# Kernel tuning notes

Measured on AMD Instinct MI355X. Metric: run time of the kernel, lower is better.

## Reference

```python
import jax, jax.numpy as jnp
import numpy as np

D = 256
NODE_COUNTS = [200000, 50000, 12000, 4000]  # n_src per block; dst of block l = NODE_COUNTS[l+1]
EDGE_COUNTS = [500000, 120000, 40000]


def setup_inputs() -> dict:
    key = jax.random.key(0)
    ks = jax.random.split(key, 16)
    x = jax.random.normal(ks[0], (NODE_COUNTS[0], D), dtype=jnp.float32)
    inp = {"x": x}
    scale = 1.0 / np.sqrt(D)
    ki = 1
    for l in range(3):
        inp[f"Wself{l}"] = jax.random.normal(ks[ki], (D, D), dtype=jnp.float32) * scale; ki += 1
        inp[f"Wneigh{l}"] = jax.random.normal(ks[ki], (D, D), dtype=jnp.float32) * scale; ki += 1
        inp[f"b{l}"] = jnp.zeros((D,), dtype=jnp.float32)
    for l in range(3):
        e = EDGE_COUNTS[l]
        inp[f"src{l}"] = jax.random.randint(ks[ki], (e,), 0, NODE_COUNTS[l]); ki += 1
        inp[f"dst{l}"] = jax.random.randint(ks[ki], (e,), 0, NODE_COUNTS[l + 1]); ki += 1
    inp["nd0"], inp["nd1"], inp["nd2"] = NODE_COUNTS[1], NODE_COUNTS[2], NODE_COUNTS[3]
    return inp


def _sage_layer(h, src, dst, n_dst, Ws, Wn, b, relu=True):
    # DGL SAGEConv('mean'): out = fc_self(h_dst) + fc_neigh(mean_{u in N(v)} h_u) + bias
    h_dst = h[:n_dst]
    msgs = h[src]                                               # [E, d] gather
    agg = jax.ops.segment_sum(msgs, dst, num_segments=n_dst)    # [n_dst, d]
    deg = jax.ops.segment_sum(jnp.ones((dst.shape[0],), h.dtype), dst, num_segments=n_dst)
    mean = agg / jnp.maximum(deg, 1.0)[:, None]
    out = h_dst @ Ws + mean @ Wn + b
    return jax.nn.relu(out) if relu else out


def reference(x, Wself0, Wneigh0, b0, Wself1, Wneigh1, b1, Wself2, Wneigh2, b2,
              src0, dst0, src1, dst1, src2, dst2, nd0, nd1, nd2):
    h = _sage_layer(x, src0, dst0, nd0, Wself0, Wneigh0, b0)
    h = _sage_layer(h, src1, dst1, nd1, Wself1, Wneigh1, b1)
    h = _sage_layer(h, src2, dst2, nd2, Wself2, Wneigh2, b2)
    return h
```

## Files before the change

### kernel.cpp

```cpp
#include <hip/hip_runtime.h>
#include <stdint.h>

#define D 256

typedef __attribute__((ext_vector_type(8))) short bf16x8;
typedef __attribute__((ext_vector_type(4))) float f32x4;

__device__ inline unsigned short f2bf(float f) {
    union { float f; uint32_t u; } v; v.f = f;
    return (unsigned short)((v.u + 0x7FFFu + ((v.u >> 16) & 1u)) >> 16);
}
__device__ inline float bf2f(unsigned short b) {
    return __uint_as_float(((uint32_t)b) << 16);
}

#define SEG0 0
#define SEG1 50176
#define SEG2 62464
#define CURTOT 66560
#define NBLK 65

__global__ __launch_bounds__(256) void convert_rows(
    const float* __restrict__ in, unsigned short* __restrict__ out, long n8)
{
    long t = (long)blockIdx.x * 256 + threadIdx.x;
    if (t >= n8) return;
    const float4* p = (const float4*)in + t * 2;
    float4 a = p[0], b = p[1];
    unsigned short r[8] = {f2bf(a.x), f2bf(a.y), f2bf(a.z), f2bf(a.w),
                           f2bf(b.x), f2bf(b.y), f2bf(b.z), f2bf(b.w)};
    *(uint4*)(out + t * 8) = *(uint4*)r;
}

struct WPtrs { const float* w[6]; };
__global__ __launch_bounds__(256) void convert_weights(
    WPtrs wp, unsigned short* __restrict__ out)
{
    int t = blockIdx.x * 256 + threadIdx.x;
    int m = t >> 16, e = t & 65535;
    int col = e >> 8, k = e & 255;
    out[t] = f2bf(wp.w[m][(k << 8) + col]);
}

__global__ __launch_bounds__(256) void count_all(
    const int* __restrict__ d0, const int* __restrict__ d1, const int* __restrict__ d2,
    int* __restrict__ cur, int E0, int E01, int Etot)
{
    int e = blockIdx.x * 256 + threadIdx.x;
    if (e >= Etot) return;
    int base, d;
    if (e < E0)       { base = SEG0; d = d0[e]; }
    else if (e < E01) { base = SEG1; d = d1[e - E0]; }
    else              { base = SEG2; d = d2[e - E01]; }
    atomicAdd(&cur[base + d], 1);
}

__global__ __launch_bounds__(256) void scan_blocks(
    int* __restrict__ cur, int* __restrict__ bsum)
{
    __shared__ int wsum[4];
    int tid = threadIdx.x, lane = tid & 63, wid = tid >> 6;
    int base = blockIdx.x * 1024 + tid * 4;
    int4 v = *(int4*)(cur + base);
    int t0 = v.x, t01 = t0 + v.y, t012 = t01 + v.z, tot = t012 + v.w;
    int incl = tot;
    #pragma unroll
    for (int ofs = 1; ofs < 64; ofs <<= 1) {
        int t = __shfl_up(incl, ofs, 64);
        if (lane >= ofs) incl += t;
    }
    if (lane == 63) wsum[wid] = incl;
    __syncthreads();
    if (tid == 0) {
        int run = 0;
        #pragma unroll
        for (int w = 0; w < 4; ++w) { int t = wsum[w]; wsum[w] = run; run += t; }
        bsum[blockIdx.x] = run;
    }
    __syncthreads();
    int texcl = wsum[wid] + incl - tot;
    v.x = texcl; v.y = texcl + t0; v.z = texcl + t01; v.w = texcl + t012;
    *(int4*)(cur + base) = v;
}

__global__ __launch_bounds__(128) void scan_bsums(
    const int* __restrict__ bsum, int* __restrict__ bscan)
{
    __shared__ int s[NBLK];
    int tid = threadIdx.x;
    if (tid < NBLK) s[tid] = bsum[tid];
    __syncthreads();
    if (tid == 0) {
        int run = 0;
        for (int b = 0; b < 49; ++b)  { int t = s[b]; s[b] = run; run += t; }
        run = 0;
        for (int b = 49; b < 61; ++b) { int t = s[b]; s[b] = run; run += t; }
        run = 0;
        for (int b = 61; b < 65; ++b) { int t = s[b]; s[b] = run; run += t; }
    }
    __syncthreads();
    if (tid < NBLK) bscan[tid] = s[tid];
}

__global__ __launch_bounds__(256) void scan_addback(
    int* __restrict__ cur, const int* __restrict__ bscan)
{
    int base = blockIdx.x * 1024 + threadIdx.x * 4;
    int add = bscan[blockIdx.x];
    int4 v = *(int4*)(cur + base);
    v.x += add; v.y += add; v.z += add; v.w += add;
    *(int4*)(cur + base) = v;
}

__global__ __launch_bounds__(256) void fill_all(
    const int* __restrict__ s0, const int* __restrict__ s1, const int* __restrict__ s2,
    const int* __restrict__ d0, const int* __restrict__ d1, const int* __restrict__ d2,
    int* __restrict__ cur, int* __restrict__ idx, int E0, int E01, int Etot)
{
    int e = blockIdx.x * 256 + threadIdx.x;
    if (e >= Etot) return;
    int base, d, s, ib;
    if (e < E0)       { base = SEG0; d = d0[e];       s = s0[e];       ib = 0; }
    else if (e < E01) { base = SEG1; d = d1[e - E0];  s = s1[e - E0];  ib = E0; }
    else              { base = SEG2; d = d2[e - E01]; s = s2[e - E01]; ib = E01; }
    int p = atomicAdd(&cur[base + d], 1);
    idx[ib + p] = s;
}

template<int BF16IN>
__global__ __launch_bounds__(256) void gather_mean_k(
    const void* __restrict__ hv, const int* __restrict__ idx,
    const int* __restrict__ curseg, unsigned short* __restrict__ mean, int M)
{
    int t = blockIdx.x * blockDim.x + threadIdx.x;
    int w = t >> 6, lane = t & 63;
    if (w >= M) return;
    int e0 = w ? curseg[w - 1] : 0;
    int e1 = curseg[w];
    float4 acc = make_float4(0.f, 0.f, 0.f, 0.f);
    int e = e0;
    if (BF16IN) {
        const unsigned short* h = (const unsigned short*)hv;
        for (; e + 1 < e1; e += 2) {
            int sa = idx[e], sb = idx[e + 1];
            ushort4 va = *(const ushort4*)(h + (size_t)sa * D + lane * 4);
            ushort4 vb = *(const ushort4*)(h + (size_t)sb * D + lane * 4);
            acc.x += bf2f(va.x) + bf2f(vb.x);
            acc.y += bf2f(va.y) + bf2f(vb.y);
            acc.z += bf2f(va.z) + bf2f(vb.z);
            acc.w += bf2f(va.w) + bf2f(vb.w);
        }
        if (e < e1) {
            int sa = idx[e];
            ushort4 va = *(const ushort4*)(h + (size_t)sa * D + lane * 4);
            acc.x += bf2f(va.x); acc.y += bf2f(va.y);
            acc.z += bf2f(va.z); acc.w += bf2f(va.w);
        }
    } else {
        const float* h = (const float*)hv;
        for (; e + 1 < e1; e += 2) {
            int sa = idx[e], sb = idx[e + 1];
            float4 va = *((const float4*)(h + (size_t)sa * D) + lane);
            float4 vb = *((const float4*)(h + (size_t)sb * D) + lane);
            acc.x += va.x + vb.x; acc.y += va.y + vb.y;
            acc.z += va.z + vb.z; acc.w += va.w + vb.w;
        }
        if (e < e1) {
            int sa = idx[e];
            float4 va = *((const float4*)(h + (size_t)sa * D) + lane);
            acc.x += va.x; acc.y += va.y; acc.z += va.z; acc.w += va.w;
        }
    }
    float r = 1.0f / fmaxf((float)(e1 - e0), 1.0f);
    ushort4 o;
    o.x = f2bf(acc.x * r); o.y = f2bf(acc.y * r);
    o.z = f2bf(acc.z * r); o.w = f2bf(acc.w * r);
    *(ushort4*)(mean + (size_t)w * D + lane * 4) = o;
}

template<int FINAL>
__global__ __launch_bounds__(256) void sage_gemm_mfma(
    const unsigned short* __restrict__ A1,
    const unsigned short* __restrict__ A2,
    const unsigned short* __restrict__ Wt1,
    const unsigned short* __restrict__ Wt2,
    const float* __restrict__ bias,
    void* __restrict__ outv,
    int M)
{
    __shared__ unsigned short As[128 * 32];
    __shared__ unsigned short Bs[128 * 32];

    int tid = threadIdx.x;
    int lane = tid & 63, wid = tid >> 6;
    int wr = wid >> 1, wc = wid & 1;
    int m0 = blockIdx.x * 128, n0 = blockIdx.y * 128;
    int l15 = lane & 15, lq = lane >> 4;

    f32x4 acc[4][4] = {};

    for (int kt = 0; kt < 16; ++kt) {
        const unsigned short* A = (kt < 8) ? A1 : A2;
        const unsigned short* B = (kt < 8) ? Wt1 : Wt2;
        int kk = (kt & 7) * 32;
        #pragma unroll
        for (int q = 0; q < 2; ++q) {
            int off16 = q * 256 + tid;
            int r = off16 >> 2, c16 = off16 & 3;
            int gr = m0 + r; if (gr >= M) gr = M - 1;
            const unsigned short* src = A + (size_t)gr * 256 + kk + c16 * 8;
            __builtin_amdgcn_global_load_lds(
                (const __attribute__((address_space(1))) void*)src,
                (__attribute__((address_space(3))) void*)(As + (q * 256 + wid * 64) * 8),
                16, 0, 0);
        }
        #pragma unroll
        for (int q = 0; q < 2; ++q) {
            int off16 = q * 256 + tid;
            int col = off16 >> 2, c16 = off16 & 3;
            const unsigned short* src = B + (size_t)(n0 + col) * 256 + kk + c16 * 8;
            __builtin_amdgcn_global_load_lds(
                (const __attribute__((address_space(1))) void*)src,
                (__attribute__((address_space(3))) void*)(Bs + (q * 256 + wid * 64) * 8),
                16, 0, 0);
        }
        __syncthreads();

        bf16x8 af[4], bfr[4];
        #pragma unroll
        for (int i = 0; i < 4; ++i) {
            int row = wr * 64 + i * 16 + l15;
            af[i] = *(const bf16x8*)(As + row * 32 + lq * 8);
            int col = wc * 64 + i * 16 + l15;
            bfr[i] = *(const bf16x8*)(Bs + col * 32 + lq * 8);
        }
        #pragma unroll
        for (int mr = 0; mr < 4; ++mr)
            #pragma unroll
            for (int nc = 0; nc < 4; ++nc)
                acc[mr][nc] = __builtin_amdgcn_mfma_f32_16x16x32_bf16(
                    af[mr], bfr[nc], acc[mr][nc], 0, 0, 0);
        __syncthreads();
    }

    #pragma unroll
    for (int nc = 0; nc < 4; ++nc) {
        int gc = n0 + wc * 64 + nc * 16 + l15;
        float bv = bias[gc];
        #pragma unroll
        for (int mr = 0; mr < 4; ++mr) {
            #pragma unroll
            for (int reg = 0; reg < 4; ++reg) {
                int gr = m0 + wr * 64 + mr * 16 + lq * 4 + reg;
                if (gr < M) {
                    float v = fmaxf(acc[mr][nc][reg] + bv, 0.f);
                    if (FINAL) ((float*)outv)[(size_t)gr * 256 + gc] = v;
                    else ((unsigned short*)outv)[(size_t)gr * 256 + gc] = f2bf(v);
                }
            }
        }
    }
}

extern "C" void kernel_launch(void* const* d_in, const int* in_sizes, int n_in,
                              void* d_out, int out_size, void* d_ws, size_t ws_size,
                              hipStream_t stream) {
    const float* x = (const float*)d_in[0];
    const float* Wself[3]  = {(const float*)d_in[1], (const float*)d_in[4], (const float*)d_in[7]};
    const float* Wneigh[3] = {(const float*)d_in[2], (const float*)d_in[5], (const float*)d_in[8]};
    const float* bias[3]   = {(const float*)d_in[3], (const float*)d_in[6], (const float*)d_in[9]};
    const int* src[3] = {(const int*)d_in[10], (const int*)d_in[12], (const int*)d_in[14]};
    const int* dst[3] = {(const int*)d_in[11], (const int*)d_in[13], (const int*)d_in[15]};
    int E[3]    = {in_sizes[10], in_sizes[12], in_sizes[14]};
    int ndst[3] = {50000, 12000, 4000};
    int E0 = E[0], E01 = E[0] + E[1], Etot = E[0] + E[1] + E[2];

    unsigned short* xb    = (unsigned short*)d_ws;
    unsigned short* h1b   = xb + (size_t)50000 * D;
    unsigned short* h2b   = h1b + (size_t)50000 * D;
    unsigned short* meanb = h2b + (size_t)12000 * D;
    unsigned short* wt    = meanb + (size_t)50000 * D;
    int* cur   = (int*)(wt + 6 * 65536);
    int* bsum  = cur + CURTOT;
    int* bscan = bsum + 80;
    int* idxa  = bscan + 80;

    WPtrs wp;
    wp.w[0] = Wself[0]; wp.w[1] = Wneigh[0];
    wp.w[2] = Wself[1]; wp.w[3] = Wneigh[1];
    wp.w[4] = Wself[2]; wp.w[5] = Wneigh[2];
    convert_weights<<<(6 * 65536) / 256, 256, 0, stream>>>(wp, wt);

    long n8 = (long)50000 * D / 8;
    convert_rows<<<(unsigned)((n8 + 255) / 256), 256, 0, stream>>>(x, xb, n8);

    hipMemsetAsync(cur, 0, CURTOT * sizeof(int), stream);
    count_all<<<(Etot + 255) / 256, 256, 0, stream>>>(dst[0], dst[1], dst[2], cur, E0, E01, Etot);
    scan_blocks<<<NBLK, 256, 0, stream>>>(cur, bsum);
    scan_bsums<<<1, 128, 0, stream>>>(bsum, bscan);
    scan_addback<<<NBLK, 256, 0, stream>>>(cur, bscan);
    fill_all<<<(Etot + 255) / 256, 256, 0, stream>>>(src[0], src[1], src[2],
        dst[0], dst[1], dst[2], cur, idxa, E0, E01, Etot);

    const unsigned short* hin_b[3] = {xb, h1b, h2b};
    void* houts[3] = {h1b, h2b, d_out};
    int segb[3] = {SEG0, SEG1, SEG2};
    int idxb[3] = {0, E0, E01};

    for (int l = 0; l < 3; ++l) {
        int M = ndst[l];
        int gt = M * 64;
        if (l == 0)
            gather_mean_k<0><<<(gt + 255) / 256, 256, 0, stream>>>(
                x, idxa + idxb[l], cur + segb[l], meanb, M);
        else
            gather_mean_k<1><<<(gt + 255) / 256, 256, 0, stream>>>(
                hin_b[l], idxa + idxb[l], cur + segb[l], meanb, M);

        dim3 grid((M + 127) / 128, 2);
        if (l < 2)
            sage_gemm_mfma<0><<<grid, 256, 0, stream>>>(hin_b[l], meanb,
                wt + (size_t)(2 * l) * 65536, wt + (size_t)(2 * l + 1) * 65536,
                bias[l], houts[l], M);
        else
            sage_gemm_mfma<1><<<grid, 256, 0, stream>>>(hin_b[l], meanb,
                wt + (size_t)(2 * l) * 65536, wt + (size_t)(2 * l + 1) * 65536,
                bias[l], houts[l], M);
    }
}
```

Before: 280.2 us.

## Fuse preprocessing kernels, convert all x to bf16, widen GEMM tile to full N

Merges weight conversion, x-to-bf16 conversion and degree counting into one launch, and converts all 200000 rows of x to bf16 instead of only the first 50000. The layer-0 gather then reads bf16 rows rather than fp32, halving the gathered bytes. The GEMM now computes all 256 output columns per block with a 128x256 tile and launch_bounds(256,2), so the A tile is loaded once instead of twice. The cost is converting 150000 extra rows, more registers per thread, and half as many GEMM blocks.

```diff
diff --git a/kernel.cpp b/kernel.cpp
--- a/kernel.cpp
+++ b/kernel.cpp
@@ -20,39 +20,43 @@
 #define CURTOT 66560
 #define NBLK 65
 
-__global__ __launch_bounds__(256) void convert_rows(
-    const float* __restrict__ in, unsigned short* __restrict__ out, long n8)
-{
-    long t = (long)blockIdx.x * 256 + threadIdx.x;
-    if (t >= n8) return;
-    const float4* p = (const float4*)in + t * 2;
-    float4 a = p[0], b = p[1];
-    unsigned short r[8] = {f2bf(a.x), f2bf(a.y), f2bf(a.z), f2bf(a.w),
-                           f2bf(b.x), f2bf(b.y), f2bf(b.z), f2bf(b.w)};
-    *(uint4*)(out + t * 8) = *(uint4*)r;
-}
-
-struct WPtrs { const float* w[6]; };
-__global__ __launch_bounds__(256) void convert_weights(
-    WPtrs wp, unsigned short* __restrict__ out)
-{
-    int t = blockIdx.x * 256 + threadIdx.x;
-    int m = t >> 16, e = t & 65535;
-    int col = e >> 8, k = e & 255;
-    out[t] = f2bf(wp.w[m][(k << 8) + col]);
-}
-
-__global__ __launch_bounds__(256) void count_all(
-    const int* __restrict__ d0, const int* __restrict__ d1, const int* __restrict__ d2,
-    int* __restrict__ cur, int E0, int E01, int Etot)
-{
-    int e = blockIdx.x * 256 + threadIdx.x;
-    if (e >= Etot) return;
-    int base, d;
-    if (e < E0)       { base = SEG0; d = d0[e]; }
-    else if (e < E01) { base = SEG1; d = d1[e - E0]; }
-    else              { base = SEG2; d = d2[e - E01]; }
-    atomicAdd(&cur[base + d], 1);
+#define WBLK 1536
+#define XBLK 25000
+
+struct PreArgs {
+    const float* w[6];
+    const float* x;
+    unsigned short* wt;
+    unsigned short* xb;
+    const int* d0; const int* d1; const int* d2;
+    int* cur;
+    int E0, E01, Etot, cblk0;
+};
+
+__global__ __launch_bounds__(256) void fused_pre(PreArgs a)
+{
+    int b = blockIdx.x;
+    if (b < WBLK) {
+        int t = b * 256 + threadIdx.x;
+        int m = t >> 16, e = t & 65535;
+        int col = e >> 8, k = e & 255;
+        a.wt[t] = f2bf(a.w[m][(k << 8) + col]);
+    } else if (b < WBLK + XBLK) {
+        long t = (long)(b - WBLK) * 256 + threadIdx.x;
+        const float4* p = (const float4*)a.x + t * 2;
+        float4 v0 = p[0], v1 = p[1];
+        unsigned short r[8] = {f2bf(v0.x), f2bf(v0.y), f2bf(v0.z), f2bf(v0.w),
+                               f2bf(v1.x), f2bf(v1.y), f2bf(v1.z), f2bf(v1.w)};
+        *(uint4*)(a.xb + t * 8) = *(uint4*)r;
+    } else {
+        int e = (b - a.cblk0) * 256 + threadIdx.x;
+        if (e >= a.Etot) return;
+        int base, d;
+        if (e < a.E0)       { base = SEG0; d = a.d0[e]; }
+        else if (e < a.E01) { base = SEG1; d = a.d1[e - a.E0]; }
+        else                { base = SEG2; d = a.d2[e - a.E01]; }
+        atomicAdd(&a.cur[base + d], 1);
+    }
 }
 
 __global__ __launch_bounds__(256) void scan_blocks(
@@ -127,9 +131,8 @@
     idx[ib + p] = s;
 }
 
-template<int BF16IN>
 __global__ __launch_bounds__(256) void gather_mean_k(
-    const void* __restrict__ hv, const int* __restrict__ idx,
+    const unsigned short* __restrict__ h, const int* __restrict__ idx,
     const int* __restrict__ curseg, unsigned short* __restrict__ mean, int M)
 {
     int t = blockIdx.x * blockDim.x + threadIdx.x;
@@ -139,37 +142,20 @@
     int e1 = curseg[w];
     float4 acc = make_float4(0.f, 0.f, 0.f, 0.f);
     int e = e0;
-    if (BF16IN) {
-        const unsigned short* h = (const unsigned short*)hv;
-        for (; e + 1 < e1; e += 2) {
-            int sa = idx[e], sb = idx[e + 1];
-            ushort4 va = *(const ushort4*)(h + (size_t)sa * D + lane * 4);
-            ushort4 vb = *(const ushort4*)(h + (size_t)sb * D + lane * 4);
-            acc.x += bf2f(va.x) + bf2f(vb.x);
-            acc.y += bf2f(va.y) + bf2f(vb.y);
-            acc.z += bf2f(va.z) + bf2f(vb.z);
-            acc.w += bf2f(va.w) + bf2f(vb.w);
-        }
-        if (e < e1) {
-            int sa = idx[e];
-            ushort4 va = *(const ushort4*)(h + (size_t)sa * D + lane * 4);
-            acc.x += bf2f(va.x); acc.y += bf2f(va.y);
-            acc.z += bf2f(va.z); acc.w += bf2f(va.w);
-        }
-    } else {
-        const float* h = (const float*)hv;
-        for (; e + 1 < e1; e += 2) {
-            int sa = idx[e], sb = idx[e + 1];
-            float4 va = *((const float4*)(h + (size_t)sa * D) + lane);
-            float4 vb = *((const float4*)(h + (size_t)sb * D) + lane);
-            acc.x += va.x + vb.x; acc.y += va.y + vb.y;
-            acc.z += va.z + vb.z; acc.w += va.w + vb.w;
-        }
-        if (e < e1) {
-            int sa = idx[e];
-            float4 va = *((const float4*)(h + (size_t)sa * D) + lane);
-            acc.x += va.x; acc.y += va.y; acc.z += va.z; acc.w += va.w;
-        }
+    for (; e + 1 < e1; e += 2) {
+        int sa = idx[e], sb = idx[e + 1];
+        ushort4 va = *(const ushort4*)(h + (size_t)sa * D + lane * 4);
+        ushort4 vb = *(const ushort4*)(h + (size_t)sb * D + lane * 4);
+        acc.x += bf2f(va.x) + bf2f(vb.x);
+        acc.y += bf2f(va.y) + bf2f(vb.y);
+        acc.z += bf2f(va.z) + bf2f(vb.z);
+        acc.w += bf2f(va.w) + bf2f(vb.w);
+    }
+    if (e < e1) {
+        int sa = idx[e];
+        ushort4 va = *(const ushort4*)(h + (size_t)sa * D + lane * 4);
+        acc.x += bf2f(va.x); acc.y += bf2f(va.y);
+        acc.z += bf2f(va.z); acc.w += bf2f(va.w);
     }
     float r = 1.0f / fmaxf((float)(e1 - e0), 1.0f);
     ushort4 o;
@@ -179,7 +165,7 @@
 }
 
 template<int FINAL>
-__global__ __launch_bounds__(256) void sage_gemm_mfma(
+__global__ __launch_bounds__(256, 2) void sage_gemm_mfma(
     const unsigned short* __restrict__ A1,
     const unsigned short* __restrict__ A2,
     const unsigned short* __restrict__ Wt1,
@@ -189,15 +175,15 @@
     int M)
 {
     __shared__ unsigned short As[128 * 32];
-    __shared__ unsigned short Bs[128 * 32];
+    __shared__ unsigned short Bs[256 * 32];
 
     int tid = threadIdx.x;
     int lane = tid & 63, wid = tid >> 6;
     int wr = wid >> 1, wc = wid & 1;
-    int m0 = blockIdx.x * 128, n0 = blockIdx.y * 128;
+    int m0 = blockIdx.x * 128;
     int l15 = lane & 15, lq = lane >> 4;
 
-    f32x4 acc[4][4] = {};
+    f32x4 acc[4][8] = {};
 
     for (int kt = 0; kt < 16; ++kt) {
         const unsigned short* A = (kt < 8) ? A1 : A2;
@@ -205,8 +191,8 @@
         int kk = (kt & 7) * 32;
         #pragma unroll
         for (int q = 0; q < 2; ++q) {
-            int off16 = q * 256 + tid;
-            int r = off16 >> 2, c16 = off16 & 3;
+            int ch = q * 256 + tid;
+            int r = ch >> 2, c16 = ch & 3;
             int gr = m0 + r; if (gr >= M) gr = M - 1;
             const unsigned short* src = A + (size_t)gr * 256 + kk + c16 * 8;
             __builtin_amdgcn_global_load_lds(
@@ -215,10 +201,10 @@
                 16, 0, 0);
         }
         #pragma unroll
-        for (int q = 0; q < 2; ++q) {
-            int off16 = q * 256 + tid;
-            int col = off16 >> 2, c16 = off16 & 3;
-            const unsigned short* src = B + (size_t)(n0 + col) * 256 + kk + c16 * 8;
+        for (int q = 0; q < 4; ++q) {
+            int ch = q * 256 + tid;
+            int col = ch >> 2, c16 = ch & 3;
+            const unsigned short* src = B + (size_t)col * 256 + kk + c16 * 8;
             __builtin_amdgcn_global_load_lds(
                 (const __attribute__((address_space(1))) void*)src,
                 (__attribute__((address_space(3))) void*)(Bs + (q * 256 + wid * 64) * 8),
@@ -226,26 +212,26 @@
         }
         __syncthreads();
 
-        bf16x8 af[4], bfr[4];
-        #pragma unroll
-        for (int i = 0; i < 4; ++i) {
-            int row = wr * 64 + i * 16 + l15;
-            af[i] = *(const bf16x8*)(As + row * 32 + lq * 8);
-            int col = wc * 64 + i * 16 + l15;
-            bfr[i] = *(const bf16x8*)(Bs + col * 32 + lq * 8);
-        }
+        bf16x8 af[4], bfr[8];
+        #pragma unroll
+        for (int i = 0; i < 4; ++i)
+            af[i] = *(const bf16x8*)(As + (wr * 64 + i * 16 + l15) * 32 + lq * 8);
+        #pragma unroll
+        for (int i = 0; i < 8; ++i)
+            bfr[i] = *(const bf16x8*)(Bs + (wc * 128 + i * 16 + l15) * 32 + lq * 8);
+
         #pragma unroll
         for (int mr = 0; mr < 4; ++mr)
             #pragma unroll
-            for (int nc = 0; nc < 4; ++nc)
+            for (int nc = 0; nc < 8; ++nc)
                 acc[mr][nc] = __builtin_amdgcn_mfma_f32_16x16x32_bf16(
                     af[mr], bfr[nc], acc[mr][nc], 0, 0, 0);
         __syncthreads();
     }
 
     #pragma unroll
-    for (int nc = 0; nc < 4; ++nc) {
-        int gc = n0 + wc * 64 + nc * 16 + l15;
+    for (int nc = 0; nc < 8; ++nc) {
+        int gc = wc * 128 + nc * 16 + l15;
         float bv = bias[gc];
         #pragma unroll
         for (int mr = 0; mr < 4; ++mr) {
@@ -276,7 +262,7 @@
     int E0 = E[0], E01 = E[0] + E[1], Etot = E[0] + E[1] + E[2];
 
     unsigned short* xb    = (unsigned short*)d_ws;
-    unsigned short* h1b   = xb + (size_t)50000 * D;
+    unsigned short* h1b   = xb + (size_t)200000 * D;
     unsigned short* h2b   = h1b + (size_t)50000 * D;
     unsigned short* meanb = h2b + (size_t)12000 * D;
     unsigned short* wt    = meanb + (size_t)50000 * D;
@@ -285,17 +271,19 @@
     int* bscan = bsum + 80;
     int* idxa  = bscan + 80;
 
-    WPtrs wp;
-    wp.w[0] = Wself[0]; wp.w[1] = Wneigh[0];
-    wp.w[2] = Wself[1]; wp.w[3] = Wneigh[1];
-    wp.w[4] = Wself[2]; wp.w[5] = Wneigh[2];
-    convert_weights<<<(6 * 65536) / 256, 256, 0, stream>>>(wp, wt);
-
-    long n8 = (long)50000 * D / 8;
-    convert_rows<<<(unsigned)((n8 + 255) / 256), 256, 0, stream>>>(x, xb, n8);
-
     hipMemsetAsync(cur, 0, CURTOT * sizeof(int), stream);
-    count_all<<<(Etot + 255) / 256, 256, 0, stream>>>(dst[0], dst[1], dst[2], cur, E0, E01, Etot);
+
+    PreArgs pa;
+    pa.w[0] = Wself[0]; pa.w[1] = Wneigh[0];
+    pa.w[2] = Wself[1]; pa.w[3] = Wneigh[1];
+    pa.w[4] = Wself[2]; pa.w[5] = Wneigh[2];
+    pa.x = x; pa.wt = wt; pa.xb = xb;
+    pa.d0 = dst[0]; pa.d1 = dst[1]; pa.d2 = dst[2];
+    pa.cur = cur; pa.E0 = E0; pa.E01 = E01; pa.Etot = Etot;
+    pa.cblk0 = WBLK + XBLK;
+    int cblk = (Etot + 255) / 256;
+    fused_pre<<<WBLK + XBLK + cblk, 256, 0, stream>>>(pa);
+
     scan_blocks<<<NBLK, 256, 0, stream>>>(cur, bsum);
     scan_bsums<<<1, 128, 0, stream>>>(bsum, bscan);
     scan_addback<<<NBLK, 256, 0, stream>>>(cur, bscan);
@@ -310,14 +298,10 @@
     for (int l = 0; l < 3; ++l) {
         int M = ndst[l];
         int gt = M * 64;
-        if (l == 0)
-            gather_mean_k<0><<<(gt + 255) / 256, 256, 0, stream>>>(
-                x, idxa + idxb[l], cur + segb[l], meanb, M);
-        else
-            gather_mean_k<1><<<(gt + 255) / 256, 256, 0, stream>>>(
-                hin_b[l], idxa + idxb[l], cur + segb[l], meanb, M);
-
-        dim3 grid((M + 127) / 128, 2);
+        gather_mean_k<<<(gt + 255) / 256, 256, 0, stream>>>(
+            hin_b[l], idxa + idxb[l], cur + segb[l], meanb, M);
+
+        dim3 grid((M + 127) / 128);
         if (l < 2)
             sage_gemm_mfma<0><<<grid, 256, 0, stream>>>(hin_b[l], meanb,
                 wt + (size_t)(2 * l) * 65536, wt + (size_t)(2 * l + 1) * 65536,
```

Result: slower. 308.2 us (+10.0%).
